# Kernel tuning notes

Hardware: AMD Instinct MI355X
Metric: run time of the kernel (lower is better)

## Reference

```python
import jax, jax.numpy as jnp
import numpy as np

EMBED_DIM = 131
SCALE = jnp.sqrt(jnp.float32(131.0))


def setup_inputs() -> dict:
    key = jax.random.key(0)
    ks = jax.random.split(key, 9)
    B, N, D = 8, 2048, EMBED_DIM
    s = 1.0 / np.sqrt(D)  # torch Linear default init scale (uniform bound)
    return {
        "query": jax.random.normal(ks[0], (B, N, D), dtype=jnp.float32),
        "key": jax.random.normal(ks[1], (B, N, D), dtype=jnp.float32),
        "value": jax.random.normal(ks[2], (B, N, D), dtype=jnp.float32),
        "Wq": jax.random.uniform(ks[3], (D, D), jnp.float32, -s, s),
        "bq": jax.random.uniform(ks[4], (D,), jnp.float32, -s, s),
        "Wk": jax.random.uniform(ks[5], (D, D), jnp.float32, -s, s),
        "bk": jax.random.uniform(ks[6], (D,), jnp.float32, -s, s),
        "Wv": jax.random.uniform(ks[7], (D, D), jnp.float32, -s, s),
        "bv": jax.random.uniform(ks[8], (D,), jnp.float32, -s, s),
    }


def reference(query, key, value, Wq, bq, Wk, bk, Wv, bv):
    # Linear projections (torch Linear: x @ W.T + b)
    Q = jnp.einsum("bnd,ed->bne", query, Wq) + bq  # [B, N, D]
    K = jnp.einsum("bnd,ed->bne", key, Wk) + bk    # [B, N, D]
    V = jnp.einsum("bnd,ed->bne", value, Wv) + bv  # [B, N, D]
    # Full attention with hardcoded scale sqrt(131)
    scores = jnp.einsum("bqd,bkd->bqk", Q, K) / SCALE  # [B, N, N]
    weights = jax.nn.softmax(scores, axis=-1)
    return jnp.einsum("bqk,bkd->bqd", weights, V)  # [B, N, D]
```

## Files before the change

kernel.cpp:

```cpp
#include <hip/hip_runtime.h>

#define B_ 8
#define N_ 2048
#define D_ 131
#define COSTR 133
#define SXSTR 164
#define CSTR 168
#define TSTR 72

typedef __attribute__((ext_vector_type(8))) short s16x8;
typedef __attribute__((ext_vector_type(16))) float f32x16;

__device__ __forceinline__ ushort f2bf(float x) {
  uint u = __float_as_uint(x);
  u += 0x7fffu + ((u >> 16) & 1u);
  return (ushort)(u >> 16);
}
__device__ __forceinline__ float bf2f(ushort h) {
  return __uint_as_float(((uint)h) << 16);
}
__device__ __forceinline__ uint bfpair(float a, float b) {
  uint ua = __float_as_uint(a);
  ua += 0x7fffu + ((ua >> 16) & 1u);
  uint ub = __float_as_uint(b);
  ub += 0x7fffu + ((ub >> 16) & 1u);
  return (ua >> 16) | (ub & 0xffff0000u);
}
__device__ __forceinline__ float f3(float a, float b, float c) {
  return fmaxf(fmaxf(a, b), c);
}
__device__ __forceinline__ float ex2(float x) { return __builtin_exp2f(x); }

__device__ __forceinline__ size_t rf32_idx(int nt, int ch, int l) {
  return ((size_t)(nt * 9 + ch) * 64 + l) * 8;
}
__device__ __forceinline__ size_t vf32_idx(int kt, int t2, int dt, int l) {
  return ((size_t)(((kt * 2) + t2) * 5 + dt) * 64 + l) * 8;
}
__device__ __forceinline__ size_t wf32_idx(int p, int h, int et, int ch, int l) {
  return ((size_t)((((p * 2 + h) * 5 + et) * 9) + ch) * 64 + l) * 8;
}

__global__ void cast_w_kernel(const float* __restrict__ Wq,
                              const float* __restrict__ Wk,
                              const float* __restrict__ Wv,
                              ushort* __restrict__ Whl) {
  const int p = blockIdx.x;
  const float* __restrict__ W = (p == 0) ? Wq : (p == 1) ? Wk : Wv;
  for (int i = threadIdx.x; i < 5 * 9 * 64; i += blockDim.x) {
    const int et = i / 576;
    const int rem = i - et * 576;
    const int ch = rem >> 6;
    const int l = rem & 63;
    const int e = et * 32 + (l & 31);
    s16x8 hi, lo;
#pragma unroll
    for (int j = 0; j < 8; ++j) {
      const int d = ch * 16 + (l >> 5) * 8 + j;
      const float val = (e < D_ && d < D_) ? W[e * D_ + d] : 0.f;
      const ushort h = f2bf(val);
      hi[j] = (short)h;
      lo[j] = (short)f2bf(val - bf2f(h));
    }
    *(s16x8*)(Whl + wf32_idx(p, 0, et, ch, l)) = hi;
    *(s16x8*)(Whl + wf32_idx(p, 1, et, ch, l)) = lo;
  }
}

template <int ET0, int NET>
__device__ __forceinline__ void compute_acc(const float* sX,
                                            const ushort* __restrict__ Whl,
                                            int p, int tg, int l,
                                            f32x16 acc[3]) {
  const int l31 = l & 31, hi = l >> 5;
#pragma unroll
  for (int ch = 0; ch < 9; ++ch) {
    const float* xp = sX + (size_t)(32 * tg + l31) * SXSTR + ch * 16 + hi * 8;
    const float4 x0 = *(const float4*)xp;
    const float4 x1 = *(const float4*)(xp + 4);
    const float xv[8] = {x0.x, x0.y, x0.z, x0.w, x1.x, x1.y, x1.z, x1.w};
    s16x8 ah, al;
#pragma unroll
    for (int j = 0; j < 8; ++j) {
      const ushort h = f2bf(xv[j]);
      ah[j] = (short)h;
      al[j] = (short)f2bf(xv[j] - bf2f(h));
    }
    s16x8 bh[NET], bl[NET];
#pragma unroll
    for (int u = 0; u < NET; ++u) {
      bh[u] = *(const s16x8*)(Whl + wf32_idx(p, 0, ET0 + u, ch, l));
      bl[u] = *(const s16x8*)(Whl + wf32_idx(p, 1, ET0 + u, ch, l));
    }
#pragma unroll
    for (int u = 0; u < NET; ++u) {
      acc[u] = __builtin_amdgcn_mfma_f32_32x32x16_bf16(ah, bh[u], acc[u], 0, 0, 0);
      acc[u] = __builtin_amdgcn_mfma_f32_32x32x16_bf16(al, bh[u], acc[u], 0, 0, 0);
      acc[u] = __builtin_amdgcn_mfma_f32_32x32x16_bf16(ah, bl[u], acc[u], 0, 0, 0);
    }
  }
}

template <int ET0, int NET>
__device__ __forceinline__ void epiQK(const f32x16 acc[3], ushort* sC,
                                      const float* sB, int tg, int l,
                                      bool scale) {
  const int l31 = l & 31, hi = l >> 5;
  const float ISC = 0.1260488539f;
#pragma unroll
  for (int u = 0; u < NET; ++u) {
    const int e = 32 * (ET0 + u) + l31;
    const float bval = sB[e];
#pragma unroll
    for (int r = 0; r < 16; ++r) {
      const int tok = 32 * tg + (r & 3) + 8 * (r >> 2) + 4 * hi;
      float val = acc[u][r] + bval;
      if (scale) val *= ISC;
      sC[(size_t)tok * CSTR + e] = f2bf(val);
    }
  }
}

template <int ET0, int NET>
__device__ __forceinline__ void epiV(const f32x16 acc[3], ushort* sT,
                                     const float* sB, int tg, int l) {
  const int l31 = l & 31, hi = l >> 5;
#pragma unroll
  for (int u = 0; u < NET; ++u) {
    const int e = 32 * (ET0 + u) + l31;
    if (e < D_) {
      const float bval = sB[e];
#pragma unroll
      for (int g = 0; g < 4; ++g) {
        const float v0 = acc[u][4 * g + 0] + bval;
        const float v1 = acc[u][4 * g + 1] + bval;
        const float v2 = acc[u][4 * g + 2] + bval;
        const float v3 = acc[u][4 * g + 3] + bval;
        uint2 pk;
        pk.x = bfpair(v0, v1);
        pk.y = bfpair(v2, v3);
        *(uint2*)(sT + (size_t)e * TSTR + 32 * tg + 8 * g + 4 * hi) = pk;
      }
    }
  }
}

__global__ __launch_bounds__(256, 3) void proj_gemm(
    const float* __restrict__ q, const float* __restrict__ k,
    const float* __restrict__ v, const float* __restrict__ bq,
    const float* __restrict__ bk, const float* __restrict__ bv,
    const ushort* __restrict__ Whl, ushort* __restrict__ Qf,
    ushort* __restrict__ Kf, ushort* __restrict__ Vf) {
  const int p = blockIdx.y;
  const float* __restrict__ x = (p == 0) ? q : (p == 1) ? k : v;
  const float* __restrict__ bias = (p == 0) ? bq : (p == 1) ? bk : bv;

  __shared__ __align__(16) char smem[64 * SXSTR * 4];
  float* sX = (float*)smem;
  ushort* sC = (ushort*)smem;
  ushort* sT = (ushort*)smem;
  __shared__ float sB[160];

  const int tid = threadIdx.x;
  const int r0 = blockIdx.x * 64;

  {
    const float* __restrict__ xbase = x + (size_t)r0 * D_;
    for (int i = tid; i < 64 * D_ / 4; i += 256) {
      const float4 v4 = *(const float4*)(xbase + i * 4);
      const float vv[4] = {v4.x, v4.y, v4.z, v4.w};
#pragma unroll
      for (int j = 0; j < 4; ++j) {
        const int nl = i * 4 + j;
        const int r = nl / D_;
        const int d = nl - r * D_;
        sX[r * SXSTR + d] = vv[j];
      }
    }
    for (int i = tid; i < 64 * 33; i += 256) {
      const int r = i / 33;
      sX[r * SXSTR + D_ + (i - r * 33)] = 0.f;
    }
  }
  if (tid < 160) sB[tid] = (tid < D_) ? bias[tid] : 0.f;
  __syncthreads();

  const int w = tid >> 6;
  const int l = tid & 63;
  const int tg = w & 1;
  const int eh = w >> 1;

  f32x16 acc[3];
  acc[0] = f32x16{};
  acc[1] = f32x16{};
  acc[2] = f32x16{};
  if (eh == 0)
    compute_acc<0, 3>(sX, Whl, p, tg, l, acc);
  else
    compute_acc<3, 2>(sX, Whl, p, tg, l, acc);

  __syncthreads();

  if (p < 2) {
    if (eh == 0)
      epiQK<0, 3>(acc, sC, sB, tg, l, p == 0);
    else
      epiQK<3, 2>(acc, sC, sB, tg, l, p == 0);
    __syncthreads();
    ushort* __restrict__ dst = (p == 0) ? Qf : Kf;
    const int nt0 = r0 >> 5;
    for (int i = tid; i < 2 * 9 * 64; i += 256) {
      const int ntl = i / 576;
      const int rem = i - ntl * 576;
      const int ch = rem >> 6;
      const int l2 = rem & 63;
      const s16x8 fr = *(const s16x8*)(sC + (size_t)(32 * ntl + (l2 & 31)) * CSTR +
                                       ch * 16 + (l2 >> 5) * 8);
      *(s16x8*)(dst + rf32_idx(nt0 + ntl, ch, l2)) = fr;
    }
  } else {
    for (int i = tid; i < 29 * 64; i += 256) {
      const int e = D_ + (i >> 6);
      sT[(size_t)e * TSTR + (i & 63)] = (e == D_) ? (ushort)0x3F80 : (ushort)0;
    }
    if (eh == 0)
      epiV<0, 3>(acc, sT, sB, tg, l);
    else
      epiV<3, 2>(acc, sT, sB, tg, l);
    __syncthreads();
    const int kt0 = r0 >> 5;
    for (int i = tid; i < 2 * 2 * 5 * 64; i += 256) {
      const int ktl = i / 640;
      const int rem = i - ktl * 640;
      const int t2 = rem / 320;
      const int rem2 = rem - t2 * 320;
      const int dt = rem2 >> 6;
      const int l2 = rem2 & 63;
      const s16x8 fr = *(const s16x8*)(sT + (size_t)(32 * dt + (l2 & 31)) * TSTR +
                                       32 * ktl + 16 * t2 + 8 * (l2 >> 5));
      *(s16x8*)(Vf + vf32_idx(kt0 + ktl, t2, dt, l2)) = fr;
    }
  }
}

__global__ __launch_bounds__(256, 2) void attn_mfma(
    const ushort* __restrict__ Qf, const ushort* __restrict__ Kf,
    const ushort* __restrict__ Vf, float* __restrict__ out) {
  const int id = blockIdx.x;
  const int b = id & 7;
  const int qg = id >> 3;
  const int tid = threadIdx.x;
  const int w = tid >> 6;
  const int l = tid & 63;
  const int l31 = l & 31;
  const int hi = l >> 5;

  __shared__ ushort sQ[9 * 64 * 8];
  __shared__ float cO[4][32][COSTR];
  __shared__ float cm[4][32];

  const int ktbase = b * 64 + w * 16;

  s16x8 kA[9], kB[9];
#pragma unroll
  for (int ch = 0; ch < 9; ++ch)
    kA[ch] = *(const s16x8*)(Kf + rf32_idx(ktbase, ch, l));
#pragma unroll
  for (int ch = 0; ch < 9; ++ch)
    kB[ch] = *(const s16x8*)(Kf + rf32_idx(ktbase + 1, ch, l));
  s16x8 va[2][5];
#pragma unroll
  for (int t2 = 0; t2 < 2; ++t2)
#pragma unroll
    for (int dt = 0; dt < 5; ++dt)
      va[t2][dt] = *(const s16x8*)(Vf + vf32_idx(ktbase, t2, dt, l));

  {
    const uint4* src = (const uint4*)(Qf + rf32_idx(b * 64 + qg, 0, 0));
    uint4* dq = (uint4*)sQ;
    for (int i = tid; i < 576; i += 256) dq[i] = src[i];
  }
  __syncthreads();

  f32x16 o[5];
#pragma unroll
  for (int dt = 0; dt < 5; ++dt) o[dt] = f32x16{};
  float mreg = -1e30f;

  auto xchg = [&](const uint pk[4]) -> s16x8 {
    const uint x0 = __shfl_xor(hi ? pk[0] : pk[2], 32, 64);
    const uint x1 = __shfl_xor(hi ? pk[1] : pk[3], 32, 64);
    uint4 u;
    u.x = hi ? x0 : pk[0];
    u.y = hi ? x1 : pk[1];
    u.z = hi ? pk[2] : x0;
    u.w = hi ? pk[3] : x1;
    return *(s16x8*)&u;
  };

#pragma unroll
  for (int i = 0; i < 8; ++i) {
    const int t0 = ktbase + 2 * i;
    f32x16 sA = f32x16{}, sB = f32x16{};
#pragma unroll
    for (int ch = 0; ch < 9; ++ch) {
      const s16x8 qc = *(const s16x8*)(sQ + (ch * 64 + l) * 8);
      sA = __builtin_amdgcn_mfma_f32_32x32x16_bf16(kA[ch], qc, sA, 0, 0, 0);
      sB = __builtin_amdgcn_mfma_f32_32x32x16_bf16(kB[ch], qc, sB, 0, 0, 0);
    }
    if (i < 7) {
#pragma unroll
      for (int ch = 0; ch < 9; ++ch)
        kA[ch] = *(const s16x8*)(Kf + rf32_idx(t0 + 2, ch, l));
#pragma unroll
      for (int ch = 0; ch < 9; ++ch)
        kB[ch] = *(const s16x8*)(Kf + rf32_idx(t0 + 3, ch, l));
    }
    {
      const float m0 = f3(sA[0], sA[1], sA[2]);
      const float m1 = f3(sA[3], sA[4], sA[5]);
      const float m2 = f3(sA[6], sA[7], sA[8]);
      const float m3 = f3(sA[9], sA[10], sA[11]);
      const float m4 = f3(sA[12], sA[13], sA[14]);
      const float m5 = f3(sA[15], sB[0], sB[1]);
      const float m6 = f3(sB[2], sB[3], sB[4]);
      const float m7 = f3(sB[5], sB[6], sB[7]);
      const float m8 = f3(sB[8], sB[9], sB[10]);
      const float m9 = f3(sB[11], sB[12], sB[13]);
      const float ma = fmaxf(sB[14], sB[15]);
      float tm = f3(f3(m0, m1, m2), f3(m3, m4, m5), f3(m6, m7, m8));
      tm = f3(tm, m9, ma);
      tm = fmaxf(tm, __shfl_xor(tm, 32, 64));
      if (__any(tm > mreg)) {
        const float mo = mreg;
        const float mn = fmaxf(mo, tm);
        mreg = mn;
        const float f = ex2(mo - mn);
        float fr[16];
#pragma unroll
        for (int r = 0; r < 16; ++r)
          fr[r] = __shfl(f, (r & 3) + 8 * (r >> 2) + 4 * hi, 64);
#pragma unroll
        for (int dt = 0; dt < 5; ++dt)
#pragma unroll
          for (int r = 0; r < 16; ++r) o[dt][r] *= fr[r];
      }
    }
    s16x8 paA[2], paB[2];
    {
      uint pk0[4], pk1[4];
#pragma unroll
      for (int wd = 0; wd < 4; ++wd) {
        pk0[wd] = bfpair(ex2(sA[2 * wd] - mreg), ex2(sA[2 * wd + 1] - mreg));
        pk1[wd] =
            bfpair(ex2(sA[8 + 2 * wd] - mreg), ex2(sA[8 + 2 * wd + 1] - mreg));
      }
      paA[0] = xchg(pk0);
      paA[1] = xchg(pk1);
#pragma unroll
      for (int wd = 0; wd < 4; ++wd) {
        pk0[wd] = bfpair(ex2(sB[2 * wd] - mreg), ex2(sB[2 * wd + 1] - mreg));
        pk1[wd] =
            bfpair(ex2(sB[8 + 2 * wd] - mreg), ex2(sB[8 + 2 * wd + 1] - mreg));
      }
      paB[0] = xchg(pk0);
      paB[1] = xchg(pk1);
    }
#pragma unroll
    for (int t2 = 0; t2 < 2; ++t2)
#pragma unroll
      for (int dt = 0; dt < 5; ++dt)
        o[dt] = __builtin_amdgcn_mfma_f32_32x32x16_bf16(paA[t2], va[t2][dt],
                                                        o[dt], 0, 0, 0);
#pragma unroll
    for (int t2 = 0; t2 < 2; ++t2)
#pragma unroll
      for (int dt = 0; dt < 5; ++dt)
        va[t2][dt] = *(const s16x8*)(Vf + vf32_idx(t0 + 1, t2, dt, l));
#pragma unroll
    for (int t2 = 0; t2 < 2; ++t2)
#pragma unroll
      for (int dt = 0; dt < 5; ++dt)
        o[dt] = __builtin_amdgcn_mfma_f32_32x32x16_bf16(paB[t2], va[t2][dt],
                                                        o[dt], 0, 0, 0);
    if (i < 7) {
#pragma unroll
      for (int t2 = 0; t2 < 2; ++t2)
#pragma unroll
        for (int dt = 0; dt < 5; ++dt)
          va[t2][dt] = *(const s16x8*)(Vf + vf32_idx(t0 + 2, t2, dt, l));
    }
  }

  if (l < 32) cm[w][l] = mreg;
#pragma unroll
  for (int dt = 0; dt < 5; ++dt) {
    const int d = 32 * dt + l31;
    if (d <= D_) {
#pragma unroll
      for (int r = 0; r < 16; ++r) {
        const int row = (r & 3) + 8 * (r >> 2) + 4 * hi;
        cO[w][row][d] = o[dt][r];
      }
    }
  }
  __syncthreads();
  for (int rr = 0; rr < 8; ++rr) {
    const int row = w * 8 + rr;
    const float m0 = cm[0][row], m1 = cm[1][row];
    const float m2 = cm[2][row], m3 = cm[3][row];
    const float M = fmaxf(fmaxf(m0, m1), fmaxf(m2, m3));
    const float e0 = ex2(m0 - M);
    const float e1 = ex2(m1 - M);
    const float e2 = ex2(m2 - M);
    const float e3 = ex2(m3 - M);
    const float lsum = cO[0][row][D_] * e0 + cO[1][row][D_] * e1 +
                       cO[2][row][D_] * e2 + cO[3][row][D_] * e3;
    const float inv = 1.f / lsum;
    float* orow = out + ((size_t)b * N_ + qg * 32 + row) * D_;
    for (int d = l; d < D_; d += 64) {
      const float val = cO[0][row][d] * e0 + cO[1][row][d] * e1 +
                        cO[2][row][d] * e2 + cO[3][row][d] * e3;
      orow[d] = val * inv;
    }
  }
}

extern "C" void kernel_launch(void* const* d_in, const int* in_sizes, int n_in,
                              void* d_out, int out_size, void* d_ws,
                              size_t ws_size, hipStream_t stream) {
  const float* q = (const float*)d_in[0];
  const float* k = (const float*)d_in[1];
  const float* v = (const float*)d_in[2];
  const float* Wq = (const float*)d_in[3];
  const float* bq = (const float*)d_in[4];
  const float* Wk = (const float*)d_in[5];
  const float* bk = (const float*)d_in[6];
  const float* Wv = (const float*)d_in[7];
  const float* bv = (const float*)d_in[8];
  float* out = (float*)d_out;

  char* wsb = (char*)d_ws;
  ushort* Qf = (ushort*)(wsb);
  ushort* Kf = (ushort*)(wsb + 4718592);
  ushort* Vf = (ushort*)(wsb + 9437184);
  ushort* Whl = (ushort*)(wsb + 14680064);

  hipLaunchKernelGGL(cast_w_kernel, dim3(3), dim3(256), 0, stream, Wq, Wk, Wv,
                     Whl);
  hipLaunchKernelGGL(proj_gemm, dim3(256, 3), dim3(256), 0, stream, q, k, v,
                     bq, bk, bv, Whl, Qf, Kf, Vf);
  hipLaunchKernelGGL(attn_mfma, dim3(512), dim3(256), 0, stream, Qf, Kf, Vf,
                     out);
}
```

Baseline: 70.07 us.

## Share staged K/V tiles in LDS across two query groups per block

```diff
diff --git a/kernel.cpp b/kernel.cpp
--- a/kernel.cpp
+++ b/kernel.cpp
@@ -243,49 +243,63 @@
   }
 }
 
-__global__ __launch_bounds__(256, 2) void attn_mfma(
+__global__ __launch_bounds__(512, 2) void attn_mfma(
     const ushort* __restrict__ Qf, const ushort* __restrict__ Kf,
     const ushort* __restrict__ Vf, float* __restrict__ out) {
   const int id = blockIdx.x;
   const int b = id & 7;
-  const int qg = id >> 3;
+  const int qblk = id >> 3;
   const int tid = threadIdx.x;
   const int w = tid >> 6;
+  const int qg = w & 1;
+  const int r = w >> 1;
   const int l = tid & 63;
   const int l31 = l & 31;
   const int hi = l >> 5;
 
-  __shared__ ushort sQ[9 * 64 * 8];
-  __shared__ float cO[4][32][COSTR];
+  __shared__ ushort kbuf[4][2][4608];
+  __shared__ ushort vbuf[4][5120];
   __shared__ float cm[4][32];
 
-  const int ktbase = b * 64 + w * 16;
-
-  s16x8 kA[9], kB[9];
+  const int qnt = b * 64 + qblk * 2 + qg;
+  s16x8 qf[9];
 #pragma unroll
   for (int ch = 0; ch < 9; ++ch)
-    kA[ch] = *(const s16x8*)(Kf + rf32_idx(ktbase, ch, l));
-#pragma unroll
-  for (int ch = 0; ch < 9; ++ch)
-    kB[ch] = *(const s16x8*)(Kf + rf32_idx(ktbase + 1, ch, l));
-  s16x8 va[2][5];
-#pragma unroll
-  for (int t2 = 0; t2 < 2; ++t2)
-#pragma unroll
-    for (int dt = 0; dt < 5; ++dt)
-      va[t2][dt] = *(const s16x8*)(Vf + vf32_idx(ktbase, t2, dt, l));
-
-  {
-    const uint4* src = (const uint4*)(Qf + rf32_idx(b * 64 + qg, 0, 0));
-    uint4* dq = (uint4*)sQ;
-    for (int i = tid; i < 576; i += 256) dq[i] = src[i];
-  }
-  __syncthreads();
-
-  f32x16 o[5];
-#pragma unroll
-  for (int dt = 0; dt < 5; ++dt) o[dt] = f32x16{};
-  float mreg = -1e30f;
+    qf[ch] = *(const s16x8*)(Qf + rf32_idx(qnt, ch, l));
+
+  const int ktbase = b * 64 + r * 16;
+
+  uint4 kr[5], vr[5];
+  auto issueK = [&](int t) {
+    const int nt = ktbase + t;
+#pragma unroll
+    for (int i = 0; i < 5; ++i) {
+      const int ch = qg ? (i < 4 ? 5 + i : 8) : i;
+      kr[i] = *(const uint4*)(Kf + rf32_idx(nt, ch, l));
+    }
+  };
+  auto issueV = [&](int t) {
+    const int kt = ktbase + t;
+#pragma unroll
+    for (int i = 0; i < 5; ++i) {
+      const int c = qg * 5 + i;
+      vr[i] = *(const uint4*)(Vf + vf32_idx(kt, c / 5, c % 5, l));
+    }
+  };
+  auto writeK = [&](int buf) {
+#pragma unroll
+    for (int i = 0; i < 5; ++i) {
+      const int ch = qg ? (i < 4 ? 5 + i : 8) : i;
+      *(uint4*)(&kbuf[r][buf][ch * 512 + l * 8]) = kr[i];
+    }
+  };
+  auto writeV = [&]() {
+#pragma unroll
+    for (int i = 0; i < 5; ++i) {
+      const int c = qg * 5 + i;
+      *(uint4*)(&vbuf[r][c * 512 + l * 8]) = vr[i];
+    }
+  };
 
   auto xchg = [&](const uint pk[4]) -> s16x8 {
     const uint x0 = __shfl_xor(hi ? pk[0] : pk[2], 32, 64);
@@ -298,38 +312,40 @@
     return *(s16x8*)&u;
   };
 
-#pragma unroll
-  for (int i = 0; i < 8; ++i) {
-    const int t0 = ktbase + 2 * i;
-    f32x16 sA = f32x16{}, sB = f32x16{};
-#pragma unroll
-    for (int ch = 0; ch < 9; ++ch) {
-      const s16x8 qc = *(const s16x8*)(sQ + (ch * 64 + l) * 8);
-      sA = __builtin_amdgcn_mfma_f32_32x32x16_bf16(kA[ch], qc, sA, 0, 0, 0);
-      sB = __builtin_amdgcn_mfma_f32_32x32x16_bf16(kB[ch], qc, sB, 0, 0, 0);
-    }
-    if (i < 7) {
-#pragma unroll
-      for (int ch = 0; ch < 9; ++ch)
-        kA[ch] = *(const s16x8*)(Kf + rf32_idx(t0 + 2, ch, l));
-#pragma unroll
-      for (int ch = 0; ch < 9; ++ch)
-        kB[ch] = *(const s16x8*)(Kf + rf32_idx(t0 + 3, ch, l));
-    }
+  f32x16 o[5];
+#pragma unroll
+  for (int dt = 0; dt < 5; ++dt) o[dt] = f32x16{};
+  float mreg = -1e30f;
+
+  issueK(0);
+  issueV(0);
+  writeK(0);
+  writeV();
+  __syncthreads();
+
+  for (int t = 0; t < 16; ++t) {
+    const int cur = t & 1;
+    const bool more = (t < 15);
+    if (more) {
+      issueK(t + 1);
+      issueV(t + 1);
+    }
+    f32x16 s = f32x16{};
     {
-      const float m0 = f3(sA[0], sA[1], sA[2]);
-      const float m1 = f3(sA[3], sA[4], sA[5]);
-      const float m2 = f3(sA[6], sA[7], sA[8]);
-      const float m3 = f3(sA[9], sA[10], sA[11]);
-      const float m4 = f3(sA[12], sA[13], sA[14]);
-      const float m5 = f3(sA[15], sB[0], sB[1]);
-      const float m6 = f3(sB[2], sB[3], sB[4]);
-      const float m7 = f3(sB[5], sB[6], sB[7]);
-      const float m8 = f3(sB[8], sB[9], sB[10]);
-      const float m9 = f3(sB[11], sB[12], sB[13]);
-      const float ma = fmaxf(sB[14], sB[15]);
-      float tm = f3(f3(m0, m1, m2), f3(m3, m4, m5), f3(m6, m7, m8));
-      tm = f3(tm, m9, ma);
+      const ushort* kb = kbuf[r][cur];
+#pragma unroll
+      for (int ch = 0; ch < 9; ++ch) {
+        const s16x8 kc = *(const s16x8*)(kb + ch * 512 + l * 8);
+        s = __builtin_amdgcn_mfma_f32_32x32x16_bf16(kc, qf[ch], s, 0, 0, 0);
+      }
+    }
+    {
+      const float a0 = f3(s[0], s[1], s[2]);
+      const float a1 = f3(s[3], s[4], s[5]);
+      const float a2 = f3(s[6], s[7], s[8]);
+      const float a3 = f3(s[9], s[10], s[11]);
+      const float a4 = f3(s[12], s[13], s[14]);
+      float tm = fmaxf(f3(a0, a1, a2), f3(a3, a4, s[15]));
       tm = fmaxf(tm, __shfl_xor(tm, 32, 64));
       if (__any(tm > mreg)) {
         const float mo = mreg;
@@ -338,90 +354,78 @@
         const float f = ex2(mo - mn);
         float fr[16];
 #pragma unroll
-        for (int r = 0; r < 16; ++r)
-          fr[r] = __shfl(f, (r & 3) + 8 * (r >> 2) + 4 * hi, 64);
+        for (int r16 = 0; r16 < 16; ++r16)
+          fr[r16] = __shfl(f, (r16 & 3) + 8 * (r16 >> 2) + 4 * hi, 64);
 #pragma unroll
         for (int dt = 0; dt < 5; ++dt)
 #pragma unroll
-          for (int r = 0; r < 16; ++r) o[dt][r] *= fr[r];
-      }
-    }
-    s16x8 paA[2], paB[2];
+          for (int r16 = 0; r16 < 16; ++r16) o[dt][r16] *= fr[r16];
+      }
+    }
+    s16x8 pa[2];
     {
       uint pk0[4], pk1[4];
 #pragma unroll
       for (int wd = 0; wd < 4; ++wd) {
-        pk0[wd] = bfpair(ex2(sA[2 * wd] - mreg), ex2(sA[2 * wd + 1] - mreg));
+        pk0[wd] = bfpair(ex2(s[2 * wd] - mreg), ex2(s[2 * wd + 1] - mreg));
         pk1[wd] =
-            bfpair(ex2(sA[8 + 2 * wd] - mreg), ex2(sA[8 + 2 * wd + 1] - mreg));
-      }
-      paA[0] = xchg(pk0);
-      paA[1] = xchg(pk1);
-#pragma unroll
-      for (int wd = 0; wd < 4; ++wd) {
-        pk0[wd] = bfpair(ex2(sB[2 * wd] - mreg), ex2(sB[2 * wd + 1] - mreg));
-        pk1[wd] =
-            bfpair(ex2(sB[8 + 2 * wd] - mreg), ex2(sB[8 + 2 * wd + 1] - mreg));
-      }
-      paB[0] = xchg(pk0);
-      paB[1] = xchg(pk1);
+            bfpair(ex2(s[8 + 2 * wd] - mreg), ex2(s[8 + 2 * wd + 1] - mreg));
+      }
+      pa[0] = xchg(pk0);
+      pa[1] = xchg(pk1);
     }
 #pragma unroll
     for (int t2 = 0; t2 < 2; ++t2)
 #pragma unroll
-      for (int dt = 0; dt < 5; ++dt)
-        o[dt] = __builtin_amdgcn_mfma_f32_32x32x16_bf16(paA[t2], va[t2][dt],
-                                                        o[dt], 0, 0, 0);
-#pragma unroll
-    for (int t2 = 0; t2 < 2; ++t2)
-#pragma unroll
-      for (int dt = 0; dt < 5; ++dt)
-        va[t2][dt] = *(const s16x8*)(Vf + vf32_idx(t0 + 1, t2, dt, l));
-#pragma unroll
-    for (int t2 = 0; t2 < 2; ++t2)
-#pragma unroll
-      for (int dt = 0; dt < 5; ++dt)
-        o[dt] = __builtin_amdgcn_mfma_f32_32x32x16_bf16(paB[t2], va[t2][dt],
-                                                        o[dt], 0, 0, 0);
-    if (i < 7) {
-#pragma unroll
-      for (int t2 = 0; t2 < 2; ++t2)
-#pragma unroll
-        for (int dt = 0; dt < 5; ++dt)
-          va[t2][dt] = *(const s16x8*)(Vf + vf32_idx(t0 + 2, t2, dt, l));
-    }
-  }
-
-  if (l < 32) cm[w][l] = mreg;
-#pragma unroll
-  for (int dt = 0; dt < 5; ++dt) {
-    const int d = 32 * dt + l31;
-    if (d <= D_) {
-#pragma unroll
-      for (int r = 0; r < 16; ++r) {
-        const int row = (r & 3) + 8 * (r >> 2) + 4 * hi;
-        cO[w][row][d] = o[dt][r];
-      }
-    }
-  }
-  __syncthreads();
-  for (int rr = 0; rr < 8; ++rr) {
-    const int row = w * 8 + rr;
-    const float m0 = cm[0][row], m1 = cm[1][row];
-    const float m2 = cm[2][row], m3 = cm[3][row];
-    const float M = fmaxf(fmaxf(m0, m1), fmaxf(m2, m3));
-    const float e0 = ex2(m0 - M);
-    const float e1 = ex2(m1 - M);
-    const float e2 = ex2(m2 - M);
-    const float e3 = ex2(m3 - M);
-    const float lsum = cO[0][row][D_] * e0 + cO[1][row][D_] * e1 +
-                       cO[2][row][D_] * e2 + cO[3][row][D_] * e3;
-    const float inv = 1.f / lsum;
-    float* orow = out + ((size_t)b * N_ + qg * 32 + row) * D_;
-    for (int d = l; d < D_; d += 64) {
-      const float val = cO[0][row][d] * e0 + cO[1][row][d] * e1 +
-                        cO[2][row][d] * e2 + cO[3][row][d] * e3;
-      orow[d] = val * inv;
+      for (int dt = 0; dt < 5; ++dt) {
+        const s16x8 vfr =
+            *(const s16x8*)(&vbuf[r][(t2 * 5 + dt) * 512 + l * 8]);
+        o[dt] = __builtin_amdgcn_mfma_f32_32x32x16_bf16(pa[t2], vfr, o[dt], 0,
+                                                        0, 0);
+      }
+    if (more) writeK(cur ^ 1);
+    __syncthreads();
+    if (more) writeV();
+    __syncthreads();
+  }
+
+  float(*cO)[32][COSTR] = (float(*)[32][COSTR]) & kbuf[0][0][0];
+#pragma unroll
+  for (int g = 0; g < 2; ++g) {
+    if (g) __syncthreads();
+    if (qg == g) {
+      if (l < 32) cm[r][l] = mreg;
+#pragma unroll
+      for (int dt = 0; dt < 5; ++dt) {
+        const int d = 32 * dt + l31;
+        if (d <= D_) {
+#pragma unroll
+          for (int r16 = 0; r16 < 16; ++r16) {
+            const int row = (r16 & 3) + 8 * (r16 >> 2) + 4 * hi;
+            cO[r][row][d] = o[dt][r16];
+          }
+        }
+      }
+    }
+    __syncthreads();
+    for (int rr = 0; rr < 4; ++rr) {
+      const int row = w * 4 + rr;
+      const float m0 = cm[0][row], m1 = cm[1][row];
+      const float m2 = cm[2][row], m3 = cm[3][row];
+      const float M = fmaxf(fmaxf(m0, m1), fmaxf(m2, m3));
+      const float e0 = ex2(m0 - M);
+      const float e1 = ex2(m1 - M);
+      const float e2 = ex2(m2 - M);
+      const float e3 = ex2(m3 - M);
+      const float lsum = cO[0][row][D_] * e0 + cO[1][row][D_] * e1 +
+                         cO[2][row][D_] * e2 + cO[3][row][D_] * e3;
+      const float inv = 1.f / lsum;
+      float* orow = out + ((size_t)b * N_ + qblk * 64 + g * 32 + row) * D_;
+      for (int d = l; d < D_; d += 64) {
+        const float val = cO[0][row][d] * e0 + cO[1][row][d] * e1 +
+                          cO[2][row][d] * e2 + cO[3][row][d] * e3;
+        orow[d] = val * inv;
+      }
     }
   }
 }
@@ -450,6 +454,6 @@
                      Whl);
   hipLaunchKernelGGL(proj_gemm, dim3(256, 3), dim3(256), 0, stream, q, k, v,
                      bq, bk, bv, Whl, Qf, Kf, Vf);
-  hipLaunchKernelGGL(attn_mfma, dim3(512), dim3(256), 0, stream, Qf, Kf, Vf,
+  hipLaunchKernelGGL(attn_mfma, dim3(256), dim3(512), 0, stream, Qf, Kf, Vf,
                      out);
 }
```

New measurement: 131.4 us. 1.87x slower.
